# Kernel optimization log

Hardware: AMD Instinct MI355X
Metric: run time of the kernel (lower is better)

## Reference

```python
import jax, jax.numpy as jnp
import numpy as np

V, D, H, O = 32000, 256, 512, 6
B, T = 128, 2048


def setup_inputs() -> dict:
    key = jax.random.key(0)
    ks = jax.random.split(key, 8)
    s = lambda k, shp, fan: jax.random.normal(k, shp, jnp.float32) / np.float32(np.sqrt(fan))
    return dict(
        token_ids=jax.random.randint(ks[0], (B, T), 0, V),
        emb=s(ks[1], (V, D), D),
        gru_wih=s(ks[2], (3 * H, D), D),
        gru_whh=s(ks[3], (3 * H, H), H),
        gru_b=jnp.zeros((3 * H,), jnp.float32),
        gru_bn=jnp.zeros((H,), jnp.float32),
        lstm_wih=s(ks[4], (4 * H, H), H),
        lstm_whh=s(ks[5], (4 * H, H), H),
        lstm_b=jnp.zeros((4 * H,), jnp.float32),
        head_w=s(ks[6], (O, H), H),
        head_b=jnp.zeros((O,), jnp.float32),
    )


def reference(token_ids, emb, gru_wih, gru_whh, gru_b, gru_bn,
              lstm_wih, lstm_whh, lstm_b, head_w, head_b):
    x = emb[token_ids]                      # (B, T, D) embedding lookup
    xs = jnp.swapaxes(x, 0, 1)              # (T, B, D) for scan over time
    h = gru_whh.shape[1]
    h0 = jnp.zeros((x.shape[0], h), x.dtype)

    def step(carry, xt):
        hg, hl, cl = carry
        # --- equinox GRUCell ---
        ig = xt @ gru_wih.T + gru_b         # (B, 3H)
        hh = hg @ gru_whh.T                 # (B, 3H)
        ir, iz, inn = jnp.split(ig, 3, axis=-1)
        hr, hz, hn = jnp.split(hh, 3, axis=-1)
        r = jax.nn.sigmoid(ir + hr)
        z = jax.nn.sigmoid(iz + hz)
        n = jnp.tanh(inn + r * (hn + gru_bn))
        hg_new = n + z * (hg - n)           # == (1-z)*n + z*hg
        # --- equinox LSTMCell (input = GRU output) ---
        lin = hg_new @ lstm_wih.T + hl @ lstm_whh.T + lstm_b  # (B, 4H)
        i_, f_, g_, o_ = jnp.split(lin, 4, axis=-1)
        c_new = jax.nn.sigmoid(f_) * cl + jax.nn.sigmoid(i_) * jnp.tanh(g_)
        h_new = jax.nn.sigmoid(o_) * jnp.tanh(c_new)
        return (hg_new, h_new, c_new), None

    (_, h_final, _), _ = jax.lax.scan(step, (h0, h0, h0), xs)
    return h_final @ head_w.T + head_b      # (B, O)
```

## Files before the change

kernel.cpp:

```cpp
#include <hip/hip_runtime.h>
#include <hip/hip_bf16.h>


typedef short v8s __attribute__((ext_vector_type(8)));
typedef float v4f __attribute__((ext_vector_type(4)));
typedef unsigned long long u64;

#define T_STEPS 2048
#define RING_OFF 8192
#define DYN_LDS 150816

#define MFMA16(a, b, c) __builtin_amdgcn_mfma_f32_16x16x32_bf16((a), (b), (c), 0, 0, 0)

__device__ __forceinline__ v4f v4zero() { v4f z = {0.f, 0.f, 0.f, 0.f}; return z; }
__device__ __forceinline__ float sigf(float x) { return 1.f / (1.f + __expf(-x)); }
__device__ __forceinline__ float tanhf_fast(float x) { return 1.f - 2.f / (1.f + __expf(2.f * x)); }

__device__ __forceinline__ ushort f2us(float v) {
  __hip_bfloat16 b = __float2bfloat16(v);
  return *reinterpret_cast<ushort*>(&b);
}
__device__ __forceinline__ float us2f(ushort u) {
  __hip_bfloat16 b;
  *reinterpret_cast<ushort*>(&b) = u;
  return __bfloat162float(b);
}
__device__ __forceinline__ void cvt_hilo(float v, ushort& h, ushort& l) {
  __hip_bfloat16 bh = __float2bfloat16(v);
  float r = v - __bfloat162float(bh);
  __hip_bfloat16 bl = __float2bfloat16(r);
  h = *reinterpret_cast<ushort*>(&bh);
  l = *reinterpret_cast<ushort*>(&bl);
}
__device__ __forceinline__ void stage4(ushort* hi, ushort* lo, const float* src) {
  float4 v = *(const float4*)src;
  float a[4] = {v.x, v.y, v.z, v.w};
#pragma unroll
  for (int j = 0; j < 4; ++j) { ushort h, l; cvt_hilo(a[j], h, l); hi[j] = h; lo[j] = l; }
}
__device__ __forceinline__ void stage4h(ushort* hi, const float* src) {
  float4 v = *(const float4*)src;
  float a[4] = {v.x, v.y, v.z, v.w};
#pragma unroll
  for (int j = 0; j < 4; ++j) hi[j] = f2us(a[j]);
}
__device__ __forceinline__ void st_wt(ushort* p, ushort v) {
  __hip_atomic_store(p, v, __ATOMIC_RELAXED, __HIP_MEMORY_SCOPE_AGENT);
}
__device__ __forceinline__ void st_row32(ushort* rowp, int r16, ushort uh) {
  unsigned v32 = (unsigned)uh;
  unsigned nb = (unsigned)__shfl_xor((int)v32, 1);
  if (!(r16 & 1)) v32 |= (nb << 16);
  unsigned hi32 = (unsigned)__shfl_xor((int)v32, 2);
  if ((r16 & 3) == 0) {
    u64 v = (u64)v32 | ((u64)hi32 << 32);
    __hip_atomic_store((u64*)(rowp + r16), v, __ATOMIC_RELAXED, __HIP_MEMORY_SCOPE_AGENT);
  }
}
__device__ __forceinline__ v8s ld_a16(const ushort* p) {
  u64 a = __hip_atomic_load((const u64*)p, __ATOMIC_RELAXED, __HIP_MEMORY_SCOPE_AGENT);
  u64 b = __hip_atomic_load((const u64*)p + 1, __ATOMIC_RELAXED, __HIP_MEMORY_SCOPE_AGENT);
  union { u64 u[2]; v8s v; } r;
  r.u[0] = a; r.u[1] = b;
  return r.v;
}

__device__ __forceinline__ int poll_ge(const int* p, int tgt, long& budget) {
  while (budget > 0) {
    if (__hip_atomic_load(p, __ATOMIC_RELAXED, __HIP_MEMORY_SCOPE_AGENT) >= tgt) return 1;
    __builtin_amdgcn_s_sleep(1);
    --budget;
  }
  return 0;
}
__device__ __forceinline__ int poll2_w0(const int* gbase, int tgtA,
                                        const int* lbase, int tgtB,
                                        int lane, long& budget) {
  const int* p = gbase;
  if (lane >= 4 && lane < 8) p = lbase + (lane - 4) * 64;
  else if (lane < 4) p = gbase + lane * 64;
  while (budget > 0) {
    int v = 0;
    if (lane < 8) v = __hip_atomic_load(p, __ATOMIC_RELAXED, __HIP_MEMORY_SCOPE_AGENT);
    v += __shfl_xor(v, 1);
    v += __shfl_xor(v, 2);
    int sa = __shfl(v, 0);
    int sb = __shfl(v, 4);
    if (sa >= tgtA && sb >= tgtB) return 1;
    __builtin_amdgcn_s_sleep(1);
    --budget;
  }
  return 0;
}

__global__ void __launch_bounds__(256, 1) rnn_persistent(
    const int* __restrict__ tok,
    const float* __restrict__ emb,
    const float* __restrict__ gwih,
    const float* __restrict__ gwhh,
    const float* __restrict__ gb,
    const float* __restrict__ gbn,
    const float* __restrict__ lwih,
    const float* __restrict__ lwhh,
    const float* __restrict__ lb,
    char* __restrict__ ws,
    int hstride, int has_lo)
{
  extern __shared__ char smem[];
  const int tid  = threadIdx.x;
  const int wgid = blockIdx.x;
  const bool is_gru = (wgid < 64);
  const int sub = is_gru ? wgid : (wgid - 64);
  const int bg  = sub & 1;
  const int cg  = sub >> 1;
  const int colbase = cg * 16;
  const int b0 = bg * 64;
  const int stripe = cg & 3;
  const int lane = tid & 63;
  const int wave = tid >> 6;
  const int quad = lane >> 4;
  const int r16  = lane & 15;

  int* cnt = (int*)ws;
  int* gru_done  = cnt + bg * 256;
  int* lstm_done = cnt + 512 + bg * 256;
  int* boot      = cnt + 1024;
  ushort* ring = (ushort*)(ws + RING_OFF);
  const int slotE = 128 * hstride;
  ushort* hlb = ring + 2 * slotE;

  const int mrow  = wave * 16 + r16;
  const int bglob = b0 + wave * 16 + quad * 4;
  const int col   = colbase + r16;
  long budget = 3000000;

  if (is_gru) {
    ushort* smemU = (ushort*)smem;
    const int WIH_HI = 0, WIH_LO = 12672, WHH_HI = 25344, WHH_LO = 50304;
    int* okf = (int*)(smem + 150528);

    for (int i = tid; i < 48 * 64; i += 256) {
      int row = i >> 6, q = (i & 63) * 4;
      int gate = row >> 4, c = colbase + (row & 15);
      stage4(&smemU[WIH_HI + row * 264 + q], &smemU[WIH_LO + row * 264 + q],
             gwih + (long)(gate * 512 + c) * 256 + q);
    }
    for (int i = tid; i < 48 * 128; i += 256) {
      int row = i >> 7, k = (i & 127) * 4;
      int gate = row >> 4, c = colbase + (row & 15);
      stage4(&smemU[WHH_HI + row * 520 + k], &smemU[WHH_LO + row * 520 + k],
             gwhh + (long)(gate * 512 + c) * 512 + k);
    }
    const float b_r  = gb[col];
    const float b_z  = gb[512 + col];
    const float b_in = gb[1024 + col];
    const float bnv  = gbn[col];
    __syncthreads();

    if (tid == 0) {
      __hip_atomic_fetch_add(boot, 1, __ATOMIC_RELEASE, __HIP_MEMORY_SCOPE_AGENT);
      long bb = 3000000;
      okf[0] = poll_ge(boot, 128, bb);
    }
    __syncthreads();
    if (!okf[0]) { if (wgid == 0 && tid == 0) st_wt(&hlb[slotE + 0], f2us(1.0e4f)); return; }

    v4f acc_r, acc_z, acc_nx;
    float hgreg[4] = {0.f, 0.f, 0.f, 0.f};
    float4 xa[16];

    auto prefetch_x = [&](int tn) {
      int ntok = tok[(b0 + mrow) * T_STEPS + tn];
      const float* xrow = emb + (long)ntok * 256;
#pragma unroll
      for (int kk = 0; kk < 8; ++kk) {
        xa[2 * kk]     = *(const float4*)(xrow + kk * 32 + quad * 8);
        xa[2 * kk + 1] = *(const float4*)(xrow + kk * 32 + quad * 8 + 4);
      }
    };
    auto accx_compute = [&]() {
      acc_r = v4zero(); acc_z = v4zero(); acc_nx = v4zero();
#pragma unroll
      for (int kk = 0; kk < 8; ++kk) {
        float xv[8] = {xa[2 * kk].x, xa[2 * kk].y, xa[2 * kk].z, xa[2 * kk].w,
                       xa[2 * kk + 1].x, xa[2 * kk + 1].y, xa[2 * kk + 1].z, xa[2 * kk + 1].w};
        v8s ahi, alo;
#pragma unroll
        for (int j = 0; j < 8; ++j) { ushort h, l; cvt_hilo(xv[j], h, l); ahi[j] = (short)h; alo[j] = (short)l; }
        const int orr = (r16) * 264 + kk * 32 + quad * 8;
        const int oz  = (16 + r16) * 264 + kk * 32 + quad * 8;
        const int on  = (32 + r16) * 264 + kk * 32 + quad * 8;
        v8s brh = *(const v8s*)&smemU[WIH_HI + orr], brl = *(const v8s*)&smemU[WIH_LO + orr];
        v8s bzh = *(const v8s*)&smemU[WIH_HI + oz],  bzl = *(const v8s*)&smemU[WIH_LO + oz];
        v8s bnh = *(const v8s*)&smemU[WIH_HI + on],  bnl = *(const v8s*)&smemU[WIH_LO + on];
        acc_r = MFMA16(ahi, brh, acc_r); acc_r = MFMA16(alo, brh, acc_r); acc_r = MFMA16(ahi, brl, acc_r);
        acc_z = MFMA16(ahi, bzh, acc_z); acc_z = MFMA16(alo, bzh, acc_z); acc_z = MFMA16(ahi, bzl, acc_z);
        acc_nx = MFMA16(ahi, bnh, acc_nx); acc_nx = MFMA16(alo, bnh, acc_nx); acc_nx = MFMA16(ahi, bnl, acc_nx);
      }
    };

    prefetch_x(0);
    accx_compute();

    for (int t = 0; t < T_STEPS; ++t) {
      if (t + 1 < T_STEPS) prefetch_x(t + 1);

      if (t > 0) {
        if (wave == 0) {
          int ok = poll2_w0(gru_done, 32 * t, lstm_done, 32 * (t - 1), lane, budget);
          if (lane == 0) okf[0] = ok;
        }
        __syncthreads();
        if (!okf[0]) { if (tid == 0) st_wt(&hlb[slotE + 2 + wgid], f2us(100.f)); break; }
      }

      v8s ahi[16], alo[16];
      if (t > 0) {
        const ushort* hrow = ring + ((t - 1) & 1) * slotE + (b0 + mrow) * hstride;
#pragma unroll
        for (int kk = 0; kk < 16; ++kk) {
          ahi[kk] = ld_a16(&hrow[kk * 32 + quad * 8]);
          if (has_lo) alo[kk] = ld_a16(&hrow[512 + kk * 32 + quad * 8]);
        }
      }

      v4f acc_nh = v4zero();
      if (t > 0) {
#pragma unroll
        for (int kk = 0; kk < 16; ++kk) {
          const int orr = (r16) * 520 + kk * 32 + quad * 8;
          const int oz  = (16 + r16) * 520 + kk * 32 + quad * 8;
          const int on  = (32 + r16) * 520 + kk * 32 + quad * 8;
          v8s brh = *(const v8s*)&smemU[WHH_HI + orr], brl = *(const v8s*)&smemU[WHH_LO + orr];
          v8s bzh = *(const v8s*)&smemU[WHH_HI + oz],  bzl = *(const v8s*)&smemU[WHH_LO + oz];
          v8s bnh = *(const v8s*)&smemU[WHH_HI + on],  bnl = *(const v8s*)&smemU[WHH_LO + on];
          acc_r = MFMA16(ahi[kk], brh, acc_r); acc_r = MFMA16(ahi[kk], brl, acc_r);
          acc_z = MFMA16(ahi[kk], bzh, acc_z); acc_z = MFMA16(ahi[kk], bzl, acc_z);
          acc_nh = MFMA16(ahi[kk], bnh, acc_nh); acc_nh = MFMA16(ahi[kk], bnl, acc_nh);
          if (has_lo) {
            acc_r = MFMA16(alo[kk], brh, acc_r);
            acc_z = MFMA16(alo[kk], bzh, acc_z);
            acc_nh = MFMA16(alo[kk], bnh, acc_nh);
          }
        }
      }

      ushort* slotT = ring + (t & 1) * slotE;
#pragma unroll
      for (int rg = 0; rg < 4; ++rg) {
        float r = sigf(acc_r[rg] + b_r);
        float z = sigf(acc_z[rg] + b_z);
        float nn = tanhf_fast(acc_nx[rg] + b_in + r * (acc_nh[rg] + bnv));
        float hnew = nn + z * (hgreg[rg] - nn);
        hgreg[rg] = hnew;
        ushort uh = f2us(hnew);
        ushort* rp = &slotT[(bglob + rg) * hstride + colbase];
        st_row32(rp, r16, uh);
        if (has_lo) st_row32(rp + 512, r16, f2us(hnew - us2f(uh)));
      }

      __syncthreads();
      if (tid == 0)
        __hip_atomic_fetch_add(gru_done + stripe * 64, 1, __ATOMIC_RELAXED, __HIP_MEMORY_SCOPE_AGENT);
      if (t + 1 < T_STEPS) accx_compute();
    }
  } else {
    ushort* smemU = (ushort*)smem;
    int* okf = (int*)(smem + 132096);

    for (int i = tid; i < 64 * 256; i += 256) {
      int row = i >> 8, k = (i & 255) * 4;
      int gate = row >> 4, c = colbase + (row & 15);
      long grow = gate * 512 + c;
      const float* src = (k < 512) ? (lwih + grow * 512 + k) : (lwhh + grow * 512 + (k - 512));
      stage4h(&smemU[row * 1032 + k], src);
    }
    const float b_i = lb[col];
    const float b_f = lb[512 + col];
    const float b_g = lb[1024 + col];
    const float b_o = lb[1536 + col];
    __syncthreads();

    if (tid == 0) {
      __hip_atomic_fetch_add(boot, 1, __ATOMIC_RELEASE, __HIP_MEMORY_SCOPE_AGENT);
      long bb = 3000000;
      okf[0] = poll_ge(boot, 128, bb);
    }
    __syncthreads();
    if (!okf[0]) { if (wgid == 64 && tid == 0) st_wt(&hlb[slotE + 1], f2us(1.0e4f)); return; }

    float creg[4] = {0.f, 0.f, 0.f, 0.f};

    for (int t = 0; t < T_STEPS; ++t) {
      if (wave == 0) {
        int ok = poll2_w0(gru_done, 32 * (t + 1), lstm_done, 32 * t, lane, budget);
        if (lane == 0) okf[0] = ok;
      }
      __syncthreads();
      if (!okf[0]) { if (tid == 0) st_wt(&hlb[slotE + 2 + wgid], f2us(100.f)); break; }

      v8s ghi[16], glo[16];
      {
        const ushort* hrow = ring + (t & 1) * slotE + (b0 + mrow) * hstride;
#pragma unroll
        for (int kk = 0; kk < 16; ++kk) {
          ghi[kk] = ld_a16(&hrow[kk * 32 + quad * 8]);
          if (has_lo) glo[kk] = ld_a16(&hrow[512 + kk * 32 + quad * 8]);
        }
      }
      v8s lhi[16], llo[16];
      const ushort* lrow = hlb + ((t - 1) & 1) * slotE + (b0 + mrow) * hstride;
      if (t > 0) {
#pragma unroll
        for (int kk = 0; kk < 16; ++kk) lhi[kk] = ld_a16(&lrow[kk * 32 + quad * 8]);
      }

      v4f ai = v4zero(), af = v4zero(), ag = v4zero(), ao = v4zero();
#pragma unroll
      for (int kk = 0; kk < 16; ++kk) {
        v8s bi = *(const v8s*)&smemU[(r16) * 1032 + kk * 32 + quad * 8];
        v8s bf = *(const v8s*)&smemU[(16 + r16) * 1032 + kk * 32 + quad * 8];
        v8s bgv = *(const v8s*)&smemU[(32 + r16) * 1032 + kk * 32 + quad * 8];
        v8s bo = *(const v8s*)&smemU[(48 + r16) * 1032 + kk * 32 + quad * 8];
        ai = MFMA16(ghi[kk], bi, ai); af = MFMA16(ghi[kk], bf, af);
        ag = MFMA16(ghi[kk], bgv, ag); ao = MFMA16(ghi[kk], bo, ao);
        if (has_lo) {
          ai = MFMA16(glo[kk], bi, ai); af = MFMA16(glo[kk], bf, af);
          ag = MFMA16(glo[kk], bgv, ag); ao = MFMA16(glo[kk], bo, ao);
        }
      }

      if (t > 0) {
        if (has_lo) {
#pragma unroll
          for (int kk = 0; kk < 16; ++kk) llo[kk] = ld_a16(&lrow[512 + kk * 32 + quad * 8]);
        }
#pragma unroll
        for (int kk = 0; kk < 16; ++kk) {
          v8s bi = *(const v8s*)&smemU[(r16) * 1032 + 512 + kk * 32 + quad * 8];
          v8s bf = *(const v8s*)&smemU[(16 + r16) * 1032 + 512 + kk * 32 + quad * 8];
          v8s bgv = *(const v8s*)&smemU[(32 + r16) * 1032 + 512 + kk * 32 + quad * 8];
          v8s bo = *(const v8s*)&smemU[(48 + r16) * 1032 + 512 + kk * 32 + quad * 8];
          ai = MFMA16(lhi[kk], bi, ai); af = MFMA16(lhi[kk], bf, af);
          ag = MFMA16(lhi[kk], bgv, ag); ao = MFMA16(lhi[kk], bo, ao);
        }
        if (has_lo) {
#pragma unroll
          for (int kk = 0; kk < 16; ++kk) {
            v8s bi = *(const v8s*)&smemU[(r16) * 1032 + 512 + kk * 32 + quad * 8];
            v8s bf = *(const v8s*)&smemU[(16 + r16) * 1032 + 512 + kk * 32 + quad * 8];
            v8s bgv = *(const v8s*)&smemU[(32 + r16) * 1032 + 512 + kk * 32 + quad * 8];
            v8s bo = *(const v8s*)&smemU[(48 + r16) * 1032 + 512 + kk * 32 + quad * 8];
            ai = MFMA16(llo[kk], bi, ai); af = MFMA16(llo[kk], bf, af);
            ag = MFMA16(llo[kk], bgv, ag); ao = MFMA16(llo[kk], bo, ao);
          }
        }
      }

      ushort* hout = hlb + (t & 1) * slotE;
#pragma unroll
      for (int rg = 0; rg < 4; ++rg) {
        float i_ = sigf(ai[rg] + b_i), f_ = sigf(af[rg] + b_f);
        float g_ = tanhf_fast(ag[rg] + b_g), o_ = sigf(ao[rg] + b_o);
        float cn = f_ * creg[rg] + i_ * g_;
        creg[rg] = cn;
        float hv = o_ * tanhf_fast(cn);
        ushort uh = f2us(hv);
        ushort* rp = &hout[(bglob + rg) * hstride + colbase];
        st_row32(rp, r16, uh);
        if (has_lo) st_row32(rp + 512, r16, f2us(hv - us2f(uh)));
      }

      __syncthreads();
      if (tid == 0)
        __hip_atomic_fetch_add(lstm_done + stripe * 64, 1, __ATOMIC_RELAXED, __HIP_MEMORY_SCOPE_AGENT);
    }
  }
}

__global__ void head_kernel(const char* __restrict__ ws,
                            const float* __restrict__ hw,
                            const float* __restrict__ hbias,
                            float* __restrict__ out,
                            int hstride, int has_lo) {
  const ushort* h1 = (const ushort*)(ws + RING_OFF) + 3 * 128 * hstride;
  const int b = blockIdx.x, l = threadIdx.x;
  const int k0 = l * 8;
  v8s hi = ld_a16(&h1[b * hstride + k0]);
  v8s lo;
  if (has_lo) lo = ld_a16(&h1[b * hstride + 512 + k0]);
  float acc[6] = {0.f, 0.f, 0.f, 0.f, 0.f, 0.f};
#pragma unroll
  for (int j = 0; j < 8; ++j) {
    float h = us2f((ushort)hi[j]);
    if (has_lo) h += us2f((ushort)lo[j]);
#pragma unroll
    for (int o = 0; o < 6; ++o) acc[o] += h * hw[o * 512 + k0 + j];
  }
#pragma unroll
  for (int o = 0; o < 6; ++o) {
    float v = acc[o];
    for (int off = 32; off > 0; off >>= 1) v += __shfl_down(v, off);
    if (l == 0) out[b * 6 + o] = v + hbias[o];
  }
}

__global__ void init_ws(int* cnt) {
  int i = blockIdx.x * blockDim.x + threadIdx.x;
  if (i < 2048)
    __hip_atomic_store(cnt + i, 0, __ATOMIC_RELAXED, __HIP_MEMORY_SCOPE_AGENT);
}

__global__ void ws_too_small_marker(float* out) {
  if (threadIdx.x == 0 && blockIdx.x == 0) out[0] = 12345.0f;
}

extern "C" void kernel_launch(void* const* d_in, const int* in_sizes, int n_in,
                              void* d_out, int out_size, void* d_ws, size_t ws_size,
                              hipStream_t stream) {
  const int*   tok  = (const int*)d_in[0];
  const float* emb  = (const float*)d_in[1];
  const float* gwih = (const float*)d_in[2];
  const float* gwhh = (const float*)d_in[3];
  const float* gb   = (const float*)d_in[4];
  const float* gbn  = (const float*)d_in[5];
  const float* lwih = (const float*)d_in[6];
  const float* lwhh = (const float*)d_in[7];
  const float* lb   = (const float*)d_in[8];
  const float* hw   = (const float*)d_in[9];
  const float* hb   = (const float*)d_in[10];

  (void)in_sizes; (void)n_in; (void)out_size;

  const size_t WS_A = (size_t)RING_OFF + 4ull * 128 * 1024 * 2;
  const size_t WS_B = (size_t)RING_OFF + 4ull * 128 * 512 * 2;
  if (ws_size < WS_B) {
    hipLaunchKernelGGL(ws_too_small_marker, dim3(1), dim3(64), 0, stream, (float*)d_out);
    return;
  }
  const int has_lo  = (ws_size >= (size_t)WS_A) ? 1 : 0;
  const int hstride = has_lo ? 1024 : 512;

  (void)hipFuncSetAttribute(reinterpret_cast<const void*>(rnn_persistent),
                            hipFuncAttributeMaxDynamicSharedMemorySize, DYN_LDS);
  hipLaunchKernelGGL(init_ws, dim3(8), dim3(256), 0, stream, (int*)d_ws);
  hipLaunchKernelGGL(rnn_persistent, dim3(128), dim3(256), DYN_LDS, stream,
                     tok, emb, gwih, gwhh, gb, gbn, lwih, lwhh, lb,
                     (char*)d_ws, hstride, has_lo);
  hipLaunchKernelGGL(head_kernel, dim3(128), dim3(64), 0, stream,
                     (const char*)d_ws, hw, hb, (float*)d_out, hstride, has_lo);
}
```

Baseline: 35.15 ms.

## Replace striped atomic step counters with per-producer epoch flags and slack polling

The cross-workgroup step barrier used fetch-add on four striped counters per batch group. It now uses one epoch word per column-group producer, written with a release store. A single wave loads all 64 epoch words in parallel and checks them with __all. The minimum lead over the target is kept as slack, so later steps can skip polling entirely. This is meant to remove atomic read-modify-write contention and shorten per-timestep synchronization latency in the persistent recurrent loop, at the cost of a different counter layout in the workspace.

```diff
diff --git a/kernel.cpp b/kernel.cpp
--- a/kernel.cpp
+++ b/kernel.cpp
@@ -73,20 +73,24 @@
   }
   return 0;
 }
-__device__ __forceinline__ int poll2_w0(const int* gbase, int tgtA,
-                                        const int* lbase, int tgtB,
-                                        int lane, long& budget) {
-  const int* p = gbase;
-  if (lane >= 4 && lane < 8) p = lbase + (lane - 4) * 64;
-  else if (lane < 4) p = gbase + lane * 64;
+__device__ __forceinline__ int pollep(const int* gepo, int ta,
+                                      const int* lepo, int tb,
+                                      int lane, long& budget, int& slack) {
+  const int* p = (lane < 32) ? (gepo + lane) : (lepo + (lane - 32));
+  const int t = (lane < 32) ? ta : tb;
   while (budget > 0) {
-    int v = 0;
-    if (lane < 8) v = __hip_atomic_load(p, __ATOMIC_RELAXED, __HIP_MEMORY_SCOPE_AGENT);
-    v += __shfl_xor(v, 1);
-    v += __shfl_xor(v, 2);
-    int sa = __shfl(v, 0);
-    int sb = __shfl(v, 4);
-    if (sa >= tgtA && sb >= tgtB) return 1;
+    int v = __hip_atomic_load(p, __ATOMIC_RELAXED, __HIP_MEMORY_SCOPE_AGENT);
+    int d = v - t;
+    if (__all(d >= 0)) {
+      int m = d;
+#pragma unroll
+      for (int off = 1; off < 64; off <<= 1) {
+        int o = __shfl_xor(m, off);
+        m = (o < m) ? o : m;
+      }
+      slack = m;
+      return 1;
+    }
     __builtin_amdgcn_s_sleep(1);
     --budget;
   }
@@ -115,16 +119,15 @@
   const int cg  = sub >> 1;
   const int colbase = cg * 16;
   const int b0 = bg * 64;
-  const int stripe = cg & 3;
   const int lane = tid & 63;
   const int wave = tid >> 6;
   const int quad = lane >> 4;
   const int r16  = lane & 15;
 
   int* cnt = (int*)ws;
-  int* gru_done  = cnt + bg * 256;
-  int* lstm_done = cnt + 512 + bg * 256;
-  int* boot      = cnt + 1024;
+  int* gru_ep  = cnt + bg * 32;
+  int* lstm_ep = cnt + 64 + bg * 32;
+  int* boot    = cnt + 128;
   ushort* ring = (ushort*)(ws + RING_OFF);
   const int slotE = 128 * hstride;
   ushort* hlb = ring + 2 * slotE;
@@ -133,6 +136,7 @@
   const int bglob = b0 + wave * 16 + quad * 4;
   const int col   = colbase + r16;
   long budget = 3000000;
+  int slack = 0;
 
   if (is_gru) {
     ushort* smemU = (ushort*)smem;
@@ -207,7 +211,9 @@
 
       if (t > 0) {
         if (wave == 0) {
-          int ok = poll2_w0(gru_done, 32 * t, lstm_done, 32 * (t - 1), lane, budget);
+          int ok = 1;
+          if (slack > 0) { --slack; }
+          else ok = pollep(gru_ep, t, lstm_ep, t - 1, lane, budget, slack);
           if (lane == 0) okf[0] = ok;
         }
         __syncthreads();
@@ -261,7 +267,7 @@
 
       __syncthreads();
       if (tid == 0)
-        __hip_atomic_fetch_add(gru_done + stripe * 64, 1, __ATOMIC_RELAXED, __HIP_MEMORY_SCOPE_AGENT);
+        __hip_atomic_store(gru_ep + cg, t + 1, __ATOMIC_RELEASE, __HIP_MEMORY_SCOPE_AGENT);
       if (t + 1 < T_STEPS) accx_compute();
     }
   } else {
@@ -293,7 +299,9 @@
 
     for (int t = 0; t < T_STEPS; ++t) {
       if (wave == 0) {
-        int ok = poll2_w0(gru_done, 32 * (t + 1), lstm_done, 32 * t, lane, budget);
+        int ok = 1;
+        if (slack > 0) { --slack; }
+        else ok = pollep(gru_ep, t + 1, lstm_ep, t, lane, budget, slack);
         if (lane == 0) okf[0] = ok;
       }
       __syncthreads();
@@ -373,7 +381,7 @@
 
       __syncthreads();
       if (tid == 0)
-        __hip_atomic_fetch_add(lstm_done + stripe * 64, 1, __ATOMIC_RELAXED, __HIP_MEMORY_SCOPE_AGENT);
+        __hip_atomic_store(lstm_ep + cg, t + 1, __ATOMIC_RELEASE, __HIP_MEMORY_SCOPE_AGENT);
     }
   }
 }
```

After: 37.06 ms. +5.4%, slower.
